# Kernel tuning notes

Measured on AMD Instinct MI355X. Metric: run time of the kernel, lower is better.

Reference implementation:

```python
import jax, jax.numpy as jnp
import numpy as np
import math

N, E = 8192, 32768
MUL_S, MUL_V = 32, 16          # 32x0e + 16x1o
DIM = MUL_S + 3 * MUL_V        # 80
NUM_RBF, HID = 16, 64
CUTOFF = 5.0
ALPHA = 5.0 / CUTOFF
# per-edge TP weight sizes (uvw paths): ss->s, s sh1->v, v sh0->v, vv->s, vv->v
O1 = MUL_S * MUL_S              # 1024
O2 = O1 + MUL_S * MUL_V         # 1536
O3 = O2 + MUL_V * MUL_V         # 1792
O4 = O3 + MUL_V * MUL_S         # 2304
WNUM = O4 + MUL_V * MUL_V       # 2560


def setup_inputs() -> dict:
    key = jax.random.key(0)
    ks = jax.random.split(key, 8)
    h = jax.random.normal(ks[0], (N, DIM), jnp.float32)
    pos = jax.random.normal(ks[1], (N, 3), jnp.float32)
    edge_index = jax.random.randint(ks[2], (2, E), 0, N)
    start = math.exp(-CUTOFF)
    means = jnp.linspace(start, 1.0, NUM_RBF).astype(jnp.float32)
    betas = jnp.full((NUM_RBF,), (2.0 / NUM_RBF * (1.0 - start)) ** -2, jnp.float32)
    W1 = jax.random.normal(ks[3], (NUM_RBF, HID), jnp.float32) / np.sqrt(NUM_RBF).astype(np.float32)
    b1 = jnp.zeros((HID,), jnp.float32)
    W2 = jax.random.normal(ks[4], (HID, WNUM), jnp.float32) / np.sqrt(HID).astype(np.float32)
    b2 = jnp.zeros((WNUM,), jnp.float32)
    Wss = jax.random.normal(ks[5], (MUL_S, MUL_S), jnp.float32)
    Wvv = jax.random.normal(ks[6], (MUL_V, MUL_V), jnp.float32)
    return {"h": h, "pos": pos, "edge_index": edge_index, "means": means,
            "betas": betas, "W1": W1, "b1": b1, "W2": W2, "b2": b2,
            "Wss": Wss, "Wvv": Wvv}


def reference(h, pos, edge_index, means, betas, W1, b1, W2, b2, Wss, Wvv):
    src, dst = edge_index[0], edge_index[1]
    vec = pos[dst] - pos[src]                           # [E,3]
    d = jnp.sqrt(jnp.sum(vec * vec, -1) + 1e-12)        # [E]
    y1 = math.sqrt(3.0) * vec / d[:, None]              # l=1 SH, component norm
    # ExpNormalSmearing with cosine cutoff
    cut = 0.5 * (jnp.cos(d * math.pi / CUTOFF) + 1.0) * (d < CUTOFF).astype(h.dtype)
    expd = jnp.exp(-ALPHA * d)[:, None]
    rbf = jnp.exp(-betas * (expd - means) ** 2) * cut[:, None]   # [E,NUM_RBF]
    # edge MLP -> per-edge TP weights
    ew = jax.nn.silu(rbf @ W1 + b1) @ W2 + b2            # [E,WNUM]
    w_ss = ew[:, :O1].reshape(E, MUL_S, MUL_S)
    w_sv = ew[:, O1:O2].reshape(E, MUL_S, MUL_V)
    w_vs = ew[:, O2:O3].reshape(E, MUL_V, MUL_V)
    w_vv0 = ew[:, O3:O4].reshape(E, MUL_V, MUL_S)
    w_vv1 = ew[:, O4:].reshape(E, MUL_V, MUL_V)
    hs = h[:, :MUL_S]                                    # [N,32]
    hv = h[:, MUL_S:].reshape(N, MUL_V, 3)               # [N,16,3]
    s_src = hs[src]                                      # [E,32]
    v_src = hv[src]                                      # [E,16,3]
    # scalar outputs: (0e x 0e -> 0e) + (1o x 1o -> 0e)
    p1 = jnp.einsum('eu,euw->ew', s_src, w_ss)
    dot = jnp.einsum('eud,ed->eu', v_src, y1) / math.sqrt(3.0)
    p4 = jnp.einsum('eu,euw->ew', dot, w_vv0)
    out_s = (p1 / math.sqrt(MUL_S) + p4 / math.sqrt(MUL_V)) / math.sqrt(2.0)
    # vector outputs: (0e x 1o -> 1o) + (1o x 0e -> 1o) + (1o x 1o -> 1o)
    p2 = jnp.einsum('eu,euw,ed->ewd', s_src, w_sv, y1)
    p3 = jnp.einsum('eud,euw->ewd', v_src, w_vs)
    cross = jnp.cross(v_src, y1[:, None, :]) / math.sqrt(2.0)
    p5 = jnp.einsum('eud,euw->ewd', cross, w_vv1)
    out_v = (p2 / math.sqrt(MUL_S) + p3 / math.sqrt(MUL_V) + p5 / math.sqrt(MUL_V)) / math.sqrt(3.0)
    msgs = jnp.concatenate([out_s, out_v.reshape(E, 3 * MUL_V)], -1)   # [E,80]
    # scatter-mean to destination nodes
    agg = jax.ops.segment_sum(msgs, dst, num_segments=N)
    cnt = jax.ops.segment_sum(jnp.ones((E,), msgs.dtype), dst, num_segments=N)
    agg = agg / jnp.maximum(cnt, 1.0)[:, None]
    # equivariant self-interaction (per-irrep channel mixing)
    si_s = hs @ Wss / math.sqrt(MUL_S)
    si_v = jnp.einsum('nud,uw->nwd', hv, Wvv) / math.sqrt(MUL_V)
    self_i = jnp.concatenate([si_s, si_v.reshape(N, 3 * MUL_V)], -1)
    return agg + self_i + h   # residual
```

## Files before the change

kernel.cpp:

```cpp
#include <hip/hip_runtime.h>
#include <math.h>

#define NN 8192
#define EE 32768
#define WN 2560
#define HID_STRIDE 72

typedef unsigned short u16;
typedef unsigned int u32;
typedef short short8 __attribute__((ext_vector_type(8)));
typedef float f32x4 __attribute__((ext_vector_type(4)));

__device__ __forceinline__ u16 f2b(float f) {
    u32 x = __float_as_uint(f);
    return (u16)((x + 0x7fffu + ((x >> 16) & 1u)) >> 16);
}

__global__ __launch_bounds__(256) void prep(const float* __restrict__ W2,
                                            u16* __restrict__ W2T,
                                            float* __restrict__ zbase) {
    const int t = threadIdx.x, b = blockIdx.x;
    const float4 z4 = {0.f, 0.f, 0.f, 0.f};
    #pragma unroll
    for (int k = 0; k < 3; ++k) {
        int i = b * 768 + k * 256 + t;
        if (i < 165888) ((float4*)zbase)[i] = z4;
    }
    if (b < 40) {
        __shared__ float tile[64][65];
        const int c0 = b << 6;
        const int tl = t & 63, th = t >> 6;
        #pragma unroll
        for (int r = 0; r < 16; ++r) {
            int kk = (r << 2) + th;
            tile[kk][tl] = W2[kk * WN + c0 + tl];
        }
        __syncthreads();
        #pragma unroll
        for (int r = 0; r < 16; ++r) {
            int c = (r << 2) + th;
            W2T[(size_t)(c0 + c) * 64 + tl] = f2b(tile[tl][c]);
        }
    }
}

__global__ __launch_bounds__(256, 4) void edge_kernel(
    const float* __restrict__ h, const float* __restrict__ pos, const int* __restrict__ ei,
    const float* __restrict__ means, const float* __restrict__ betas,
    const float* __restrict__ W1, const float* __restrict__ b1,
    const u16* __restrict__ W2T, const float* __restrict__ b2,
    float* __restrict__ agg, float* __restrict__ cnt)
{
    __shared__ alignas(16) char sbuf[28416];
    float (*sh_ss)[33]    = (float (*)[33])(sbuf);
    float (*sh_dot)[17]   = (float (*)[17])(sbuf + 4224);
    float (*sh_v)[68]     = (float (*)[68])(sbuf + 6400);
    float (*sh_cross)[68] = (float (*)[68])(sbuf + 15104);
    u16*  sh_hidb         = (u16*)(sbuf + 23808);
    float (*redS)[32][33] = (float (*)[32][33])(sbuf);
    float (*redQ)[32][17] = (float (*)[32][17])(sbuf + 16896);
    float (*redV)[32][49] = (float (*)[32][49])(sbuf);

    __shared__ float sh_y1[32][3];
    __shared__ float sh_geo[32][2];
    __shared__ int   sh_src[32];
    __shared__ int   sh_dst[32];

    const int t = threadIdx.x;

    if (t < 32) {
        const int eg = (blockIdx.x << 5) + t;
        const int si = ei[eg];
        const int di = ei[EE + eg];
        float ax = pos[si*3+0], ay = pos[si*3+1], az = pos[si*3+2];
        float bx = pos[di*3+0], by = pos[di*3+1], bz = pos[di*3+2];
        float vx = bx-ax, vy = by-ay, vz = bz-az;
        float d = sqrtf(vx*vx + vy*vy + vz*vz + 1e-12f);
        float invd = 1.7320508075688772f / d;
        sh_y1[t][0] = vx*invd; sh_y1[t][1] = vy*invd; sh_y1[t][2] = vz*invd;
        sh_geo[t][0] = expf(-d);
        sh_geo[t][1] = (d < 5.0f) ? 0.5f*(cosf(d*0.6283185307179586f) + 1.0f) : 0.0f;
        sh_src[t] = si; sh_dst[t] = di;
    }
    __syncthreads();

    {
        const int e = t >> 3, r = t & 7;
        const float expd = sh_geo[e][0], cut = sh_geo[e][1];
        float rbf[16];
        #pragma unroll
        for (int k = 0; k < 16; ++k) {
            float td = expd - means[k];
            rbf[k] = expf(-betas[k]*td*td) * cut;
        }
        short8 pk;
        #pragma unroll
        for (int jj = 0; jj < 8; ++jj) {
            int j = (r << 3) + jj;
            float a = b1[j];
            #pragma unroll
            for (int k = 0; k < 16; ++k) a += rbf[k] * W1[(k<<6) + j];
            float s = a / (1.0f + expf(-a));
            pk[jj] = (short)f2b(s);
        }
        *(short8*)&sh_hidb[e*HID_STRIDE + (r<<3)] = pk;

        const int srcn = sh_src[e];
        const float* hrow = h + srcn*80;
        const float y1x = sh_y1[e][0], y1y = sh_y1[e][1], y1z = sh_y1[e][2];
        #pragma unroll
        for (int i = 0; i < 4; ++i) { int u = (r<<2)+i; sh_ss[e][u] = 0.125f * hrow[u]; }
        #pragma unroll
        for (int i = 0; i < 2; ++i) {
            int u = (r<<1)+i;
            float v0 = hrow[32+u*3+0];
            float v1 = hrow[32+u*3+1];
            float v2 = hrow[32+u*3+2];
            sh_v[e][(u<<2)+0] = v0 * 0.14433756729740643f;
            sh_v[e][(u<<2)+1] = v1 * 0.14433756729740643f;
            sh_v[e][(u<<2)+2] = v2 * 0.14433756729740643f;
            sh_dot[e][u] = (v0*y1x + v1*y1y + v2*y1z) * 0.10206207261596574f;
            sh_cross[e][(u<<2)+0] = (v1*y1z - v2*y1y) * 0.10206207261596574f;
            sh_cross[e][(u<<2)+1] = (v2*y1x - v0*y1z) * 0.10206207261596574f;
            sh_cross[e][(u<<2)+2] = (v0*y1y - v1*y1x) * 0.10206207261596574f;
        }
    }
    __syncthreads();

    const int ln = t & 63, wv = t >> 6;
    const int quad = ln >> 4, lm = ln & 15;
    short8 af[2][2];
    #pragma unroll
    for (int mt = 0; mt < 2; ++mt)
        #pragma unroll
        for (int ks = 0; ks < 2; ++ks)
            af[mt][ks] = *(const short8*)&sh_hidb[(mt*16+lm)*HID_STRIDE + (ks<<5) + (quad<<3)];

    float accS[2][4][2];
    float accQ[2][4];
    float accV[2][4][3];
    #pragma unroll
    for (int mt = 0; mt < 2; ++mt)
        #pragma unroll
        for (int r = 0; r < 4; ++r) {
            accS[mt][r][0] = accS[mt][r][1] = 0.f;
            accQ[mt][r] = 0.f;
            accV[mt][r][0] = accV[mt][r][1] = accV[mt][r][2] = 0.f;
        }

    #pragma unroll 1
    for (int cj = 0; cj < 20; ++cj) {
        short8 bfr[2][2];
        float b2v[2];
        #pragma unroll
        for (int i = 0; i < 2; ++i) {
            const int coll = (((wv<<1)+i)<<4) + lm;
            const int col  = (cj<<7) + coll;
            bfr[i][0] = *(const short8*)(W2T + (size_t)col*64 + (quad<<3));
            bfr[i][1] = *(const short8*)(W2T + (size_t)col*64 + 32 + (quad<<3));
            b2v[i] = b2[col];
        }
        f32x4 d[2][2];
        #pragma unroll
        for (int i = 0; i < 2; ++i) {
            d[i][0] = (f32x4){0.f,0.f,0.f,0.f};
            d[i][1] = (f32x4){0.f,0.f,0.f,0.f};
            d[i][0] = __builtin_amdgcn_mfma_f32_16x16x32_bf16(af[0][0], bfr[i][0], d[i][0], 0,0,0);
            d[i][0] = __builtin_amdgcn_mfma_f32_16x16x32_bf16(af[0][1], bfr[i][1], d[i][0], 0,0,0);
            d[i][1] = __builtin_amdgcn_mfma_f32_16x16x32_bf16(af[1][0], bfr[i][0], d[i][1], 0,0,0);
            d[i][1] = __builtin_amdgcn_mfma_f32_16x16x32_bf16(af[1][1], bfr[i][1], d[i][1], 0,0,0);
            d[i][0] += b2v[i];
            d[i][1] += b2v[i];
        }

        if (cj < 8) {
            const int j = (cj<<2) + wv;
            #pragma unroll
            for (int mt = 0; mt < 2; ++mt)
                #pragma unroll
                for (int r = 0; r < 4; ++r) {
                    const int e = (mt<<4) + (quad<<2) + r;
                    float s0 = sh_ss[e][j];
                    accS[mt][r][0] += s0*d[0][mt][r];
                    accS[mt][r][1] += s0*d[1][mt][r];
                }
        } else if (cj < 12) {
            const int ub = ((cj-8)<<3) + (wv<<1);
            #pragma unroll
            for (int mt = 0; mt < 2; ++mt)
                #pragma unroll
                for (int r = 0; r < 4; ++r) {
                    const int e = (mt<<4) + (quad<<2) + r;
                    accQ[mt][r] += sh_ss[e][ub]*d[0][mt][r] + sh_ss[e][ub+1]*d[1][mt][r];
                }
        } else if (cj < 14) {
            const int ub = ((cj-12)<<3) + (wv<<1);
            #pragma unroll
            for (int mt = 0; mt < 2; ++mt)
                #pragma unroll
                for (int r = 0; r < 4; ++r) {
                    const int e = (mt<<4) + (quad<<2) + r;
                    #pragma unroll
                    for (int i = 0; i < 2; ++i) {
                        const float4 vv = *(const float4*)&sh_v[e][(ub+i)<<2];
                        float ew = d[i][mt][r];
                        accV[mt][r][0] += vv.x * ew;
                        accV[mt][r][1] += vv.y * ew;
                        accV[mt][r][2] += vv.z * ew;
                    }
                }
        } else if (cj < 18) {
            const int j = ((cj-14)<<2) + wv;
            #pragma unroll
            for (int mt = 0; mt < 2; ++mt)
                #pragma unroll
                for (int r = 0; r < 4; ++r) {
                    const int e = (mt<<4) + (quad<<2) + r;
                    float s0 = sh_dot[e][j];
                    accS[mt][r][0] += s0*d[0][mt][r];
                    accS[mt][r][1] += s0*d[1][mt][r];
                }
        } else {
            const int ub = ((cj-18)<<3) + (wv<<1);
            #pragma unroll
            for (int mt = 0; mt < 2; ++mt)
                #pragma unroll
                for (int r = 0; r < 4; ++r) {
                    const int e = (mt<<4) + (quad<<2) + r;
                    #pragma unroll
                    for (int i = 0; i < 2; ++i) {
                        const float4 cc = *(const float4*)&sh_cross[e][(ub+i)<<2];
                        float ew = d[i][mt][r];
                        accV[mt][r][0] += cc.x * ew;
                        accV[mt][r][1] += cc.y * ew;
                        accV[mt][r][2] += cc.z * ew;
                    }
                }
        }
    }

    __syncthreads();
    #pragma unroll
    for (int mt = 0; mt < 2; ++mt)
        #pragma unroll
        for (int r = 0; r < 4; ++r) {
            const int e = (mt<<4) + (quad<<2) + r;
            redS[wv][e][lm]    = accS[mt][r][0];
            redS[wv][e][lm+16] = accS[mt][r][1];
            redQ[wv][e][lm]    = accQ[mt][r];
        }
    __syncthreads();

    #pragma unroll
    for (int k = 0; k < 4; ++k) {
        int p = t + (k<<8); int e = p >> 5; int w = p & 31;
        float v = redS[0][e][w] + redS[1][e][w] + redS[2][e][w] + redS[3][e][w];
        atomicAdd(&agg[sh_dst[e]*80 + w], v);
    }
    float q2v[2];
    #pragma unroll
    for (int k = 0; k < 2; ++k) {
        int p = t + (k<<8); int e = p >> 4; int w = p & 15;
        q2v[k] = redQ[0][e][w] + redQ[1][e][w] + redQ[2][e][w] + redQ[3][e][w];
    }
    __syncthreads();

    #pragma unroll
    for (int mt = 0; mt < 2; ++mt)
        #pragma unroll
        for (int r = 0; r < 4; ++r) {
            const int e = (mt<<4) + (quad<<2) + r;
            redV[wv][e][lm*3+0] = accV[mt][r][0];
            redV[wv][e][lm*3+1] = accV[mt][r][1];
            redV[wv][e][lm*3+2] = accV[mt][r][2];
        }
    __syncthreads();

    #pragma unroll
    for (int k = 0; k < 2; ++k) {
        int p = t + (k<<8); int e = p >> 4; int w = p & 15;
        #pragma unroll
        for (int dd = 0; dd < 3; ++dd) {
            int m = w*3 + dd;
            float pv = redV[0][e][m] + redV[1][e][m] + redV[2][e][m] + redV[3][e][m];
            float val = pv + q2v[k] * sh_y1[e][dd] * 0.8164965809277261f;
            atomicAdd(&agg[sh_dst[e]*80 + 32 + m], val);
        }
    }
    if (t < 32) atomicAdd(&cnt[sh_dst[t]], 1.0f);
}

__global__ __launch_bounds__(256, 8) void node_kernel(
    const float* __restrict__ h, const float* __restrict__ Wss, const float* __restrict__ Wvv,
    const float* __restrict__ agg, const float* __restrict__ cnt,
    float* __restrict__ out)
{
    const int b = blockIdx.x, t = threadIdx.x;
    if (b < 1024) {
        const int idx = (b<<8) + t;
        const int n = idx >> 5, j = idx & 31;
        const float* hrow = h + n*80;
        float si = 0.f;
        #pragma unroll
        for (int u = 0; u < 32; ++u) si += hrow[u] * Wss[(u<<5)+j];
        float a = agg[n*80+j] / fmaxf(cnt[n], 1.0f);
        out[n*80+j] = a + si*0.17677669529663687f + hrow[j];
    } else {
        const int idx = ((b-1024)<<8) + t;
        const int n = idx / 48, m = idx - n*48;
        const int w = m/3, d = m - w*3;
        const float* hrow = h + n*80;
        float si = 0.f;
        #pragma unroll
        for (int u = 0; u < 16; ++u) si += hrow[32+u*3+d] * Wvv[(u<<4)+w];
        float a = agg[n*80+32+m] / fmaxf(cnt[n], 1.0f);
        out[n*80+32+m] = a + si*0.25f + hrow[32+m];
    }
}

extern "C" void kernel_launch(void* const* d_in, const int* in_sizes, int n_in,
                              void* d_out, int out_size, void* d_ws, size_t ws_size,
                              hipStream_t stream) {
    const float* h     = (const float*)d_in[0];
    const float* pos   = (const float*)d_in[1];
    const int*   ei    = (const int*)d_in[2];
    const float* means = (const float*)d_in[3];
    const float* betas = (const float*)d_in[4];
    const float* W1    = (const float*)d_in[5];
    const float* b1    = (const float*)d_in[6];
    const float* W2    = (const float*)d_in[7];
    const float* b2    = (const float*)d_in[8];
    const float* Wss   = (const float*)d_in[9];
    const float* Wvv   = (const float*)d_in[10];

    float* agg = (float*)d_ws;
    float* cnt = agg + (size_t)NN*80;
    u16*   W2T = (u16*)(cnt + NN);

    hipLaunchKernelGGL(prep, dim3(256), dim3(256), 0, stream, W2, W2T, agg);
    hipLaunchKernelGGL(edge_kernel, dim3(EE/32), dim3(256), 0, stream,
                       h, pos, ei, means, betas, W1, b1, W2T, b2, agg, cnt);
    hipLaunchKernelGGL(node_kernel, dim3(2560), dim3(256), 0, stream,
                       h, Wss, Wvv, agg, cnt, (float*)d_out);
}
```

Before: 169.9 us.

## Split edge chunk loop into per-path phases with LDS atomic reduction

The single 20-iteration loop with branch dispatch is split into separate loops per TP path. Each loop keeps only its own accumulators live, which reduces register pressure. Cross-wave reductions now use LDS atomicAdd into dedicated zero-initialised outS/outV buffers instead of staged reduction arrays, removing two block barriers. The cost is extra LDS, LDS atomic contention across the four waves, and an initial zeroing pass.

```diff
diff --git a/kernel.cpp b/kernel.cpp
--- a/kernel.cpp
+++ b/kernel.cpp
@@ -57,16 +57,24 @@
     float (*sh_v)[68]     = (float (*)[68])(sbuf + 6400);
     float (*sh_cross)[68] = (float (*)[68])(sbuf + 15104);
     u16*  sh_hidb         = (u16*)(sbuf + 23808);
-    float (*redS)[32][33] = (float (*)[32][33])(sbuf);
-    float (*redQ)[32][17] = (float (*)[32][17])(sbuf + 16896);
-    float (*redV)[32][49] = (float (*)[32][49])(sbuf);
-
+
+    __shared__ float outS[32][33];
+    __shared__ float outV[32][49];
     __shared__ float sh_y1[32][3];
     __shared__ float sh_geo[32][2];
     __shared__ int   sh_src[32];
     __shared__ int   sh_dst[32];
 
     const int t = threadIdx.x;
+
+    {
+        float* z = &outS[0][0];
+        #pragma unroll
+        for (int i = 0; i < 5; ++i) { int p = t + (i<<8); if (p < 1056) z[p] = 0.f; }
+        float* z2 = &outV[0][0];
+        #pragma unroll
+        for (int i = 0; i < 7; ++i) { int p = t + (i<<8); if (p < 1568) z2[p] = 0.f; }
+    }
 
     if (t < 32) {
         const int eg = (blockIdx.x << 5) + t;
@@ -136,56 +144,58 @@
         for (int ks = 0; ks < 2; ++ks)
             af[mt][ks] = *(const short8*)&sh_hidb[(mt*16+lm)*HID_STRIDE + (ks<<5) + (quad<<3)];
 
-    float accS[2][4][2];
-    float accQ[2][4];
-    float accV[2][4][3];
-    #pragma unroll
-    for (int mt = 0; mt < 2; ++mt)
-        #pragma unroll
-        for (int r = 0; r < 4; ++r) {
-            accS[mt][r][0] = accS[mt][r][1] = 0.f;
-            accQ[mt][r] = 0.f;
-            accV[mt][r][0] = accV[mt][r][1] = accV[mt][r][2] = 0.f;
-        }
-
-    #pragma unroll 1
-    for (int cj = 0; cj < 20; ++cj) {
-        short8 bfr[2][2];
-        float b2v[2];
+    const u16* W2Tq = W2T + (quad<<3);
+    auto halfchunk = [&](int cj, f32x4 (&d)[2][2]) {
         #pragma unroll
         for (int i = 0; i < 2; ++i) {
-            const int coll = (((wv<<1)+i)<<4) + lm;
-            const int col  = (cj<<7) + coll;
-            bfr[i][0] = *(const short8*)(W2T + (size_t)col*64 + (quad<<3));
-            bfr[i][1] = *(const short8*)(W2T + (size_t)col*64 + 32 + (quad<<3));
-            b2v[i] = b2[col];
-        }
-        f32x4 d[2][2];
-        #pragma unroll
-        for (int i = 0; i < 2; ++i) {
-            d[i][0] = (f32x4){0.f,0.f,0.f,0.f};
-            d[i][1] = (f32x4){0.f,0.f,0.f,0.f};
-            d[i][0] = __builtin_amdgcn_mfma_f32_16x16x32_bf16(af[0][0], bfr[i][0], d[i][0], 0,0,0);
-            d[i][0] = __builtin_amdgcn_mfma_f32_16x16x32_bf16(af[0][1], bfr[i][1], d[i][0], 0,0,0);
-            d[i][1] = __builtin_amdgcn_mfma_f32_16x16x32_bf16(af[1][0], bfr[i][0], d[i][1], 0,0,0);
-            d[i][1] = __builtin_amdgcn_mfma_f32_16x16x32_bf16(af[1][1], bfr[i][1], d[i][1], 0,0,0);
-            d[i][0] += b2v[i];
-            d[i][1] += b2v[i];
-        }
-
-        if (cj < 8) {
+            const int col = (cj<<7) + (wv<<5) + (i<<4) + lm;
+            const short8 b0  = *(const short8*)(W2Tq + (size_t)col*64);
+            const short8 b1v = *(const short8*)(W2Tq + (size_t)col*64 + 32);
+            const float bb = b2[col];
+            f32x4 a0 = {0.f,0.f,0.f,0.f}, a1 = {0.f,0.f,0.f,0.f};
+            a0 = __builtin_amdgcn_mfma_f32_16x16x32_bf16(af[0][0], b0,  a0, 0,0,0);
+            a0 = __builtin_amdgcn_mfma_f32_16x16x32_bf16(af[0][1], b1v, a0, 0,0,0);
+            a1 = __builtin_amdgcn_mfma_f32_16x16x32_bf16(af[1][0], b0,  a1, 0,0,0);
+            a1 = __builtin_amdgcn_mfma_f32_16x16x32_bf16(af[1][1], b1v, a1, 0,0,0);
+            d[i][0] = a0 + bb;
+            d[i][1] = a1 + bb;
+        }
+    };
+
+    {
+        float accS[2][4][2] = {};
+        #pragma unroll 1
+        for (int cj = 0; cj < 8; ++cj) {
+            f32x4 d[2][2];
+            halfchunk(cj, d);
             const int j = (cj<<2) + wv;
             #pragma unroll
             for (int mt = 0; mt < 2; ++mt)
                 #pragma unroll
                 for (int r = 0; r < 4; ++r) {
                     const int e = (mt<<4) + (quad<<2) + r;
-                    float s0 = sh_ss[e][j];
+                    const float s0 = sh_ss[e][j];
                     accS[mt][r][0] += s0*d[0][mt][r];
                     accS[mt][r][1] += s0*d[1][mt][r];
                 }
-        } else if (cj < 12) {
-            const int ub = ((cj-8)<<3) + (wv<<1);
+        }
+        #pragma unroll
+        for (int mt = 0; mt < 2; ++mt)
+            #pragma unroll
+            for (int r = 0; r < 4; ++r) {
+                const int e = (mt<<4) + (quad<<2) + r;
+                atomicAdd(&outS[e][lm],    accS[mt][r][0]);
+                atomicAdd(&outS[e][lm+16], accS[mt][r][1]);
+            }
+    }
+
+    {
+        float accQ[2][4] = {};
+        #pragma unroll 1
+        for (int cj = 0; cj < 4; ++cj) {
+            f32x4 d[2][2];
+            halfchunk(cj + 8, d);
+            const int ub = (cj<<3) + (wv<<1);
             #pragma unroll
             for (int mt = 0; mt < 2; ++mt)
                 #pragma unroll
@@ -193,8 +203,26 @@
                     const int e = (mt<<4) + (quad<<2) + r;
                     accQ[mt][r] += sh_ss[e][ub]*d[0][mt][r] + sh_ss[e][ub+1]*d[1][mt][r];
                 }
-        } else if (cj < 14) {
-            const int ub = ((cj-12)<<3) + (wv<<1);
+        }
+        #pragma unroll
+        for (int mt = 0; mt < 2; ++mt)
+            #pragma unroll
+            for (int r = 0; r < 4; ++r) {
+                const int e = (mt<<4) + (quad<<2) + r;
+                const float q = accQ[mt][r] * 0.8164965809277261f;
+                atomicAdd(&outV[e][3*lm+0], q * sh_y1[e][0]);
+                atomicAdd(&outV[e][3*lm+1], q * sh_y1[e][1]);
+                atomicAdd(&outV[e][3*lm+2], q * sh_y1[e][2]);
+            }
+    }
+
+    {
+        float accV[2][4][3] = {};
+        #pragma unroll 1
+        for (int cj = 0; cj < 2; ++cj) {
+            f32x4 d[2][2];
+            halfchunk(cj + 12, d);
+            const int ub = (cj<<3) + (wv<<1);
             #pragma unroll
             for (int mt = 0; mt < 2; ++mt)
                 #pragma unroll
@@ -203,25 +231,44 @@
                     #pragma unroll
                     for (int i = 0; i < 2; ++i) {
                         const float4 vv = *(const float4*)&sh_v[e][(ub+i)<<2];
-                        float ew = d[i][mt][r];
+                        const float ew = d[i][mt][r];
                         accV[mt][r][0] += vv.x * ew;
                         accV[mt][r][1] += vv.y * ew;
                         accV[mt][r][2] += vv.z * ew;
                     }
                 }
-        } else if (cj < 18) {
-            const int j = ((cj-14)<<2) + wv;
-            #pragma unroll
-            for (int mt = 0; mt < 2; ++mt)
-                #pragma unroll
-                for (int r = 0; r < 4; ++r) {
-                    const int e = (mt<<4) + (quad<<2) + r;
-                    float s0 = sh_dot[e][j];
-                    accS[mt][r][0] += s0*d[0][mt][r];
-                    accS[mt][r][1] += s0*d[1][mt][r];
-                }
-        } else {
-            const int ub = ((cj-18)<<3) + (wv<<1);
+        }
+        {
+            float accS[2][4][2] = {};
+            #pragma unroll 1
+            for (int cj = 0; cj < 4; ++cj) {
+                f32x4 d[2][2];
+                halfchunk(cj + 14, d);
+                const int j = (cj<<2) + wv;
+                #pragma unroll
+                for (int mt = 0; mt < 2; ++mt)
+                    #pragma unroll
+                    for (int r = 0; r < 4; ++r) {
+                        const int e = (mt<<4) + (quad<<2) + r;
+                        const float s0 = sh_dot[e][j];
+                        accS[mt][r][0] += s0*d[0][mt][r];
+                        accS[mt][r][1] += s0*d[1][mt][r];
+                    }
+            }
+            #pragma unroll
+            for (int mt = 0; mt < 2; ++mt)
+                #pragma unroll
+                for (int r = 0; r < 4; ++r) {
+                    const int e = (mt<<4) + (quad<<2) + r;
+                    atomicAdd(&outS[e][lm],    accS[mt][r][0]);
+                    atomicAdd(&outS[e][lm+16], accS[mt][r][1]);
+                }
+        }
+        #pragma unroll 1
+        for (int cj = 0; cj < 2; ++cj) {
+            f32x4 d[2][2];
+            halfchunk(cj + 18, d);
+            const int ub = (cj<<3) + (wv<<1);
             #pragma unroll
             for (int mt = 0; mt < 2; ++mt)
                 #pragma unroll
@@ -230,62 +277,35 @@
                     #pragma unroll
                     for (int i = 0; i < 2; ++i) {
                         const float4 cc = *(const float4*)&sh_cross[e][(ub+i)<<2];
-                        float ew = d[i][mt][r];
+                        const float ew = d[i][mt][r];
                         accV[mt][r][0] += cc.x * ew;
                         accV[mt][r][1] += cc.y * ew;
                         accV[mt][r][2] += cc.z * ew;
                     }
                 }
         }
-    }
-
-    __syncthreads();
-    #pragma unroll
-    for (int mt = 0; mt < 2; ++mt)
-        #pragma unroll
-        for (int r = 0; r < 4; ++r) {
-            const int e = (mt<<4) + (quad<<2) + r;
-            redS[wv][e][lm]    = accS[mt][r][0];
-            redS[wv][e][lm+16] = accS[mt][r][1];
-            redQ[wv][e][lm]    = accQ[mt][r];
-        }
+        #pragma unroll
+        for (int mt = 0; mt < 2; ++mt)
+            #pragma unroll
+            for (int r = 0; r < 4; ++r) {
+                const int e = (mt<<4) + (quad<<2) + r;
+                atomicAdd(&outV[e][3*lm+0], accV[mt][r][0]);
+                atomicAdd(&outV[e][3*lm+1], accV[mt][r][1]);
+                atomicAdd(&outV[e][3*lm+2], accV[mt][r][2]);
+            }
+    }
+
     __syncthreads();
 
     #pragma unroll
     for (int k = 0; k < 4; ++k) {
         int p = t + (k<<8); int e = p >> 5; int w = p & 31;
-        float v = redS[0][e][w] + redS[1][e][w] + redS[2][e][w] + redS[3][e][w];
-        atomicAdd(&agg[sh_dst[e]*80 + w], v);
-    }
-    float q2v[2];
+        atomicAdd(&agg[sh_dst[e]*80 + w], outS[e][w]);
+    }
     #pragma unroll
-    for (int k = 0; k < 2; ++k) {
-        int p = t + (k<<8); int e = p >> 4; int w = p & 15;
-        q2v[k] = redQ[0][e][w] + redQ[1][e][w] + redQ[2][e][w] + redQ[3][e][w];
-    }
-    __syncthreads();
-
-    #pragma unroll
-    for (int mt = 0; mt < 2; ++mt)
-        #pragma unroll
-        for (int r = 0; r < 4; ++r) {
-            const int e = (mt<<4) + (quad<<2) + r;
-            redV[wv][e][lm*3+0] = accV[mt][r][0];
-            redV[wv][e][lm*3+1] = accV[mt][r][1];
-            redV[wv][e][lm*3+2] = accV[mt][r][2];
-        }
-    __syncthreads();
-
-    #pragma unroll
-    for (int k = 0; k < 2; ++k) {
-        int p = t + (k<<8); int e = p >> 4; int w = p & 15;
-        #pragma unroll
-        for (int dd = 0; dd < 3; ++dd) {
-            int m = w*3 + dd;
-            float pv = redV[0][e][m] + redV[1][e][m] + redV[2][e][m] + redV[3][e][m];
-            float val = pv + q2v[k] * sh_y1[e][dd] * 0.8164965809277261f;
-            atomicAdd(&agg[sh_dst[e]*80 + 32 + m], val);
-        }
+    for (int k = 0; k < 6; ++k) {
+        int p = t + (k<<8); int e = p/48; int m = p - e*48;
+        atomicAdd(&agg[sh_dst[e]*80 + 32 + m], outV[e][m]);
     }
     if (t < 32) atomicAdd(&cnt[sh_dst[t]], 1.0f);
 }
```

After: 217.1 us. 27.8% more time.
